# Kernel optimization log

Hardware: AMD Instinct MI355X
Metric: run time of the kernel (lower is better)

Reference implementation:

```python
import jax, jax.numpy as jnp
import numpy as np

NU, NI, E = 100000, 100000, 500000  # users, items, edges per edge type
DIN, DH, DOUT = 128, 256, 128


def setup_inputs() -> dict:
    key = jax.random.key(0)
    ks = jax.random.split(key, 18)
    f = lambda k, s: jax.random.normal(k, s, dtype=jnp.float32) * 0.02
    inp = {
        # node embedding tables (x_dict defaults to embedding weights)
        'emb_user': f(ks[0], (NU, DIN)),
        'emb_item': f(ks[1], (NI, DIN)),
        # conv1 params: relation user->item (dst=item) and item->user (dst=user)
        'W1_self_ui': f(ks[2], (DIN, DH)), 'W1_neigh_ui': f(ks[3], (DIN, DH)), 'b1_ui': jnp.zeros((DH,), jnp.float32),
        'W1_self_iu': f(ks[4], (DIN, DH)), 'W1_neigh_iu': f(ks[5], (DIN, DH)), 'b1_iu': jnp.zeros((DH,), jnp.float32),
        # conv2 params
        'W2_self_ui': f(ks[6], (DH, DOUT)), 'W2_neigh_ui': f(ks[7], (DH, DOUT)), 'b2_ui': jnp.zeros((DOUT,), jnp.float32),
        'W2_self_iu': f(ks[8], (DH, DOUT)), 'W2_neigh_iu': f(ks[9], (DH, DOUT)), 'b2_iu': jnp.zeros((DOUT,), jnp.float32),
        # edge lists: e1 = user->item edges, e2 = item->user edges
        'e1_src': jax.random.randint(ks[10], (E,), 0, NU),
        'e1_dst': jax.random.randint(ks[11], (E,), 0, NI),
        'e2_src': jax.random.randint(ks[12], (E,), 0, NI),
        'e2_dst': jax.random.randint(ks[13], (E,), 0, NU),
    }
    return inp


def _sage(h_src, h_dst, e_src, e_dst, W_self, W_neigh, b, n_dst):
    # DGL SAGEConv('mean'): fc_self(h_dst) + fc_neigh(mean_neighbors(h_src)) + bias
    msg = h_src[e_src]                                   # [E, d] gather
    ssum = jax.ops.segment_sum(msg, e_dst, num_segments=n_dst)          # [n_dst, d]
    deg = jax.ops.segment_sum(jnp.ones((e_src.shape[0], 1), h_src.dtype), e_dst, num_segments=n_dst)
    mean = ssum / jnp.maximum(deg, 1.0)                  # zero in-degree -> 0
    return h_dst @ W_self + mean @ W_neigh + b


def reference(emb_user, emb_item,
              W1_self_ui, W1_neigh_ui, b1_ui, W1_self_iu, W1_neigh_iu, b1_iu,
              W2_self_ui, W2_neigh_ui, b2_ui, W2_self_iu, W2_neigh_iu, b2_iu,
              e1_src, e1_dst, e2_src, e2_dst):
    # layer 1 (HeteroGraphConv: each ntype receives from exactly one relation)
    h1_item = jax.nn.leaky_relu(_sage(emb_user, emb_item, e1_src, e1_dst, W1_self_ui, W1_neigh_ui, b1_ui, NI))
    h1_user = jax.nn.leaky_relu(_sage(emb_item, emb_user, e2_src, e2_dst, W1_self_iu, W1_neigh_iu, b1_iu, NU))
    # layer 2
    h2_item = _sage(h1_user, h1_item, e1_src, e1_dst, W2_self_ui, W2_neigh_ui, b2_ui, NI)
    h2_user = _sage(h1_item, h1_user, e2_src, e2_dst, W2_self_iu, W2_neigh_iu, b2_iu, NU)
    return (h2_user, h2_item)
```

## Files before the change

### kernel.cpp

```cpp
#include <hip/hip_runtime.h>
#include <stdint.h>

typedef unsigned short u16;
typedef unsigned int   u32;
typedef __attribute__((ext_vector_type(8))) short bf16x8;
typedef __attribute__((ext_vector_type(4))) float f32x4;
typedef __attribute__((ext_vector_type(2))) float f32x2;
typedef __attribute__((ext_vector_type(8))) unsigned short u16x8;

constexpr int NUc = 100000;
constexpr int NIc = 100000;
constexpr int Ec  = 500000;
constexpr int Mrows = 100000;
constexpr int NB  = (100000 + 255) / 256;

__device__ __forceinline__ u16 f2bf(float f) {
  u32 u = __float_as_uint(f);
  u += 0x7fffu + ((u >> 16) & 1u);
  return (u16)(u >> 16);
}

__global__ void hist_kernel(const int* __restrict__ e1_dst, const int* __restrict__ e2_dst,
                            int* __restrict__ ideg1, int* __restrict__ ideg2,
                            int* __restrict__ rank1, int* __restrict__ rank2) {
  int i = blockIdx.x * blockDim.x + threadIdx.x;
  const int stride = gridDim.x * blockDim.x;
  for (; i < 2 * Ec; i += stride) {
    if (i < Ec) rank1[i] = atomicAdd(&ideg1[e1_dst[i]], 1);
    else        rank2[i - Ec] = atomicAdd(&ideg2[e2_dst[i - Ec]], 1);
  }
}

constexpr int PREP_B = 4096;
__global__ void prep_cast(const float* __restrict__ eu, const float* __restrict__ ei,
                          const float* __restrict__ W1s_ui, const float* __restrict__ W1n_ui,
                          const float* __restrict__ W1s_iu, const float* __restrict__ W1n_iu,
                          const float* __restrict__ W2s_ui, const float* __restrict__ W2n_ui,
                          const float* __restrict__ W2s_iu, const float* __restrict__ W2n_iu,
                          u16* __restrict__ ue, u16* __restrict__ ie,
                          u16* __restrict__ Wt1_ui, u16* __restrict__ Wt1_iu,
                          u16* __restrict__ Wt2c_u, u16* __restrict__ Wt2c_i) {
  constexpr int N4 = NUc * 128 / 4;
  constexpr int TOT = 2 * N4 + 262144;
  int i = blockIdx.x * blockDim.x + threadIdx.x;
  const int stride = PREP_B * 256;
  for (int t = i; t < TOT; t += stride) {
    if (t < 2 * N4) {
      const float* src = (t < N4) ? eu : ei;
      u16* dst = (t < N4) ? ue : ie;
      int c = (t < N4) ? t : t - N4;
      f32x4 v = __builtin_nontemporal_load(reinterpret_cast<const f32x4*>(src) + c);
      ushort4 o;
      o.x = f2bf(v.x); o.y = f2bf(v.y); o.z = f2bf(v.z); o.w = f2bf(v.w);
      reinterpret_cast<ushort4*>(dst)[c] = o;
    } else {
      int j = t - 2 * N4;
      if (j < 131072) {
        const float* Ws = (j < 65536) ? W1s_ui : W1s_iu;
        const float* Wn = (j < 65536) ? W1n_ui : W1n_iu;
        u16* dst = (j < 65536) ? Wt1_ui : Wt1_iu;
        int q = j & 65535;
        int n = q >> 8, k = q & 255;
        dst[q] = f2bf(k < 128 ? Ws[k * 256 + n] : Wn[(k - 128) * 256 + n]);
      } else {
        int q = j - 131072;
        int which = q >> 16;
        int s = q & 65535;
        int c = s >> 8, k = s & 255;
        float v;
        if (which == 0) v = (c < 128) ? W2n_ui[k * 128 + c] : W2s_iu[k * 128 + (c - 128)];
        else            v = (c < 128) ? W2n_iu[k * 128 + c] : W2s_ui[k * 128 + (c - 128)];
        u16* dst = which ? Wt2c_i : Wt2c_u;
        dst[s] = f2bf(v);
      }
    }
  }
}

__global__ void block_reduce2(const int* __restrict__ ideg1, const int* __restrict__ ideg2,
                              int* __restrict__ bsum1, int* __restrict__ bsum2, int n) {
  const int* deg = blockIdx.y ? ideg2 : ideg1;
  int* bsum = blockIdx.y ? bsum2 : bsum1;
  __shared__ int s[256];
  int t = threadIdx.x, i = blockIdx.x * 256 + t;
  s[t] = (i < n) ? deg[i] : 0;
  __syncthreads();
  for (int st = 128; st > 0; st >>= 1) { if (t < st) s[t] += s[t + st]; __syncthreads(); }
  if (t == 0) bsum[blockIdx.x] = s[0];
}

__global__ void scan_bsums2(const int* __restrict__ bsum1, const int* __restrict__ bsum2,
                            int* __restrict__ bscan1, int* __restrict__ bscan2, int nb) {
  const int* bsum = blockIdx.x ? bsum2 : bsum1;
  int* bscan = blockIdx.x ? bscan2 : bscan1;
  __shared__ int s[512];
  int t = threadIdx.x;
  int v0 = (t < nb) ? bsum[t] : 0;
  s[t] = v0;
  __syncthreads();
  for (int d = 1; d < 512; d <<= 1) {
    int v = (t >= d) ? s[t - d] : 0;
    __syncthreads();
    s[t] += v;
    __syncthreads();
  }
  if (t < nb) bscan[t] = s[t] - v0;
}

__global__ void scan_blocks2(const int* __restrict__ ideg1, const int* __restrict__ ideg2,
                             const int* __restrict__ bscan1, const int* __restrict__ bscan2,
                             int* __restrict__ off1, int* __restrict__ off2, int n) {
  const int* deg = blockIdx.y ? ideg2 : ideg1;
  const int* bscan = blockIdx.y ? bscan2 : bscan1;
  int* off = blockIdx.y ? off2 : off1;
  __shared__ int s[256];
  int t = threadIdx.x, i = blockIdx.x * 256 + t;
  int d = (i < n) ? deg[i] : 0;
  s[t] = d;
  __syncthreads();
  for (int st = 1; st < 256; st <<= 1) {
    int v = (t >= st) ? s[t - st] : 0;
    __syncthreads();
    s[t] += v;
    __syncthreads();
  }
  if (i < n) off[i] = bscan[blockIdx.x] + s[t] - d;
  if (i == 0) off[n] = Ec;
}

__global__ void fill_csr_kernel(const int* __restrict__ e1_src, const int* __restrict__ e1_dst,
                                const int* __restrict__ e2_src, const int* __restrict__ e2_dst,
                                const int* __restrict__ rank1, const int* __restrict__ rank2,
                                const int* __restrict__ off1, const int* __restrict__ off2,
                                int* __restrict__ csr1, int* __restrict__ csr2) {
  int i = blockIdx.x * blockDim.x + threadIdx.x;
  const int stride = gridDim.x * blockDim.x;
  for (; i < 2 * Ec; i += stride) {
    if (i < Ec) {
      int d = __builtin_nontemporal_load(e1_dst + i);
      int r = __builtin_nontemporal_load(rank1 + i);
      csr1[off1[d] + r] = __builtin_nontemporal_load(e1_src + i);
    } else {
      int e = i - Ec;
      int d = __builtin_nontemporal_load(e2_dst + e);
      int r = __builtin_nontemporal_load(rank2 + e);
      csr2[off2[d] + r] = __builtin_nontemporal_load(e2_src + e);
    }
  }
}

template<int FINAL>
__global__ __launch_bounds__(256) void gather_blk(
    const u16* __restrict__ fA, const int* __restrict__ offA, const int* __restrict__ csrA,
    const u16* __restrict__ sA, void* __restrict__ outA,
    const u16* __restrict__ fB, const int* __restrict__ offB, const int* __restrict__ csrB,
    const u16* __restrict__ sB, void* __restrict__ outB)
{
  constexpr int ROWS = 64;
  constexpr int CAP  = 1536;
  constexpr int NBLK = (100000 + ROWS - 1) / ROWS;
  __shared__ int s_off[ROWS + 1];
  __shared__ int s_csr[CAP];

  const int b = blockIdx.x;
  const u16* f; const int* off; const int* csr; const u16* sf; void* out; int r0;
  if (b < NBLK) { f = fA; off = offA; csr = csrA; sf = sA; out = outA; r0 = b * ROWS; }
  else          { f = fB; off = offB; csr = csrB; sf = sB; out = outB; r0 = (b - NBLK) * ROWS; }

  const int tid = threadIdx.x;
  if (tid <= ROWS) s_off[tid] = off[min(r0 + tid, 100000)];
  __syncthreads();
  const int j0 = s_off[0];
  const int nE = s_off[ROWS] - j0;
  const bool inLds = (nE <= CAP);
  if (inLds) {
    for (int j = tid; j < nE; j += 256) s_csr[j] = csr[j0 + j];
  }
  __syncthreads();

  const int w = tid >> 6, lane = tid & 63;
  const int colb = lane << 1;
  for (int rr = w; rr < ROWS; rr += 4) {
    const int r = r0 + rr;
    if (r >= 100000) break;
    const int a0 = s_off[rr], a1 = s_off[rr + 1];
    float ax = 0.f, ay = 0.f;
    if (inLds) {
      int tl = a0 - j0;
      const int el = a1 - j0;
      for (; tl + 4 <= el; tl += 4) {
        int s0 = s_csr[tl], s1 = s_csr[tl + 1], s2 = s_csr[tl + 2], s3 = s_csr[tl + 3];
        u32 v0 = *reinterpret_cast<const u32*>(f + (size_t)s0 * 128 + colb);
        u32 v1 = *reinterpret_cast<const u32*>(f + (size_t)s1 * 128 + colb);
        u32 v2 = *reinterpret_cast<const u32*>(f + (size_t)s2 * 128 + colb);
        u32 v3 = *reinterpret_cast<const u32*>(f + (size_t)s3 * 128 + colb);
        ax += __uint_as_float(v0 << 16) + __uint_as_float(v1 << 16)
            + __uint_as_float(v2 << 16) + __uint_as_float(v3 << 16);
        ay += __uint_as_float(v0 & 0xffff0000u) + __uint_as_float(v1 & 0xffff0000u)
            + __uint_as_float(v2 & 0xffff0000u) + __uint_as_float(v3 & 0xffff0000u);
      }
      for (; tl < el; ++tl) {
        int s0 = s_csr[tl];
        u32 v0 = *reinterpret_cast<const u32*>(f + (size_t)s0 * 128 + colb);
        ax += __uint_as_float(v0 << 16);
        ay += __uint_as_float(v0 & 0xffff0000u);
      }
    } else {
      int t = a0;
      for (; t + 4 <= a1; t += 4) {
        int s0 = csr[t], s1 = csr[t + 1], s2 = csr[t + 2], s3 = csr[t + 3];
        u32 v0 = *reinterpret_cast<const u32*>(f + (size_t)s0 * 128 + colb);
        u32 v1 = *reinterpret_cast<const u32*>(f + (size_t)s1 * 128 + colb);
        u32 v2 = *reinterpret_cast<const u32*>(f + (size_t)s2 * 128 + colb);
        u32 v3 = *reinterpret_cast<const u32*>(f + (size_t)s3 * 128 + colb);
        ax += __uint_as_float(v0 << 16) + __uint_as_float(v1 << 16)
            + __uint_as_float(v2 << 16) + __uint_as_float(v3 << 16);
        ay += __uint_as_float(v0 & 0xffff0000u) + __uint_as_float(v1 & 0xffff0000u)
            + __uint_as_float(v2 & 0xffff0000u) + __uint_as_float(v3 & 0xffff0000u);
      }
      for (; t < a1; ++t) {
        int s0 = csr[t];
        u32 v0 = *reinterpret_cast<const u32*>(f + (size_t)s0 * 128 + colb);
        ax += __uint_as_float(v0 << 16);
        ay += __uint_as_float(v0 & 0xffff0000u);
      }
    }
    float rs = 1.0f / fmaxf((float)(a1 - a0), 1.0f);
    if (FINAL) {
      u32 sv = __builtin_nontemporal_load(
          reinterpret_cast<const u32*>(sf + (size_t)r * 128 + colb));
      f32x2 o;
      o.x = ax * rs + __uint_as_float(sv << 16);
      o.y = ay * rs + __uint_as_float(sv & 0xffff0000u);
      __builtin_nontemporal_store(o, reinterpret_cast<f32x2*>((float*)out + (size_t)r * 128 + colb));
    } else {
      u32 o = (u32)f2bf(ax * rs) | ((u32)f2bf(ay * rs) << 16);
      *reinterpret_cast<u32*>((u16*)out + (size_t)r * 128 + colb) = o;
    }
  }
}

__device__ __forceinline__ void glds16(const void* g, void* l) {
  __builtin_amdgcn_global_load_lds((const __attribute__((address_space(1))) void*)g,
                                   (__attribute__((address_space(3))) void*)l, 16, 0, 0);
}

__global__ __launch_bounds__(256) void fused_gemm(
    const u16* __restrict__ Xa, const u16* __restrict__ Sa,
    const u16* __restrict__ W1a, const float* __restrict__ b1a,
    const u16* __restrict__ W2a, const float* __restrict__ b2a,
    u16* __restrict__ proja, u16* __restrict__ selfa,
    const u16* __restrict__ Xb, const u16* __restrict__ Sb,
    const u16* __restrict__ W1b, const float* __restrict__ b1b,
    const u16* __restrict__ W2b, const float* __restrict__ b2b,
    u16* __restrict__ projb, u16* __restrict__ selfb,
    int M)
{
  constexpr int K = 256, BK = 32, BM = 64;
  __shared__ __align__(16) u16 As[BM * BK];
  __shared__ __align__(16) u16 Bs[256 * BK];
  __shared__ __align__(16) u16 slab[BM * 256];

  const bool zb = (blockIdx.z != 0);
  const u16* X   = zb ? Xb : Xa;
  const u16* S   = zb ? Sb : Sa;
  const u16* W1  = zb ? W1b : W1a;
  const float* b1 = zb ? b1b : b1a;
  const u16* W2  = zb ? W2b : W2a;
  const float* b2 = zb ? b2b : b2a;
  u16* proj  = zb ? projb : proja;
  u16* selfp = zb ? selfb : selfa;

  const int tid  = threadIdx.x;
  const int lane = tid & 63;
  const int w    = tid >> 6;
  const int gr0  = blockIdx.x * BM;
  const int rl   = tid >> 2;
  const int sslot = tid & 3;

  f32x4 acc[4][4];
  #pragma unroll
  for (int m = 0; m < 4; ++m)
    #pragma unroll
    for (int n = 0; n < 4; ++n) acc[m][n] = (f32x4){0.f, 0.f, 0.f, 0.f};

  for (int kt = 0; kt < K; kt += BK) {
    const u16* At = (kt >= 128) ? S : X;
    const int kbase = kt & 127;
    {
      int swz = (sslot ^ ((rl >> 1) & 3)) << 3;
      int grow = gr0 + rl; grow = grow < M ? grow : M - 1;
      glds16(At + (size_t)grow * 128 + kbase + swz, As + (size_t)(w * 16) * BK);
    }
    #pragma unroll
    for (int h = 0; h < 4; ++h) {
      int rb = h * 64 + rl;
      int swz = (sslot ^ ((rb >> 1) & 3)) << 3;
      glds16(W1 + (size_t)rb * K + kt + swz, Bs + (size_t)(h * 64 + w * 16) * BK);
    }
    __syncthreads();

    bf16x8 af[4], bfr[4];
    #pragma unroll
    for (int m = 0; m < 4; ++m) {
      int row = m * 16 + (lane & 15);
      int idx = (row << 5) + ((((lane >> 4) ^ ((row >> 1) & 3))) << 3);
      af[m] = *reinterpret_cast<const bf16x8*>(As + idx);
    }
    #pragma unroll
    for (int n = 0; n < 4; ++n) {
      int row = w * 64 + n * 16 + (lane & 15);
      int idx = (row << 5) + ((((lane >> 4) ^ ((row >> 1) & 3))) << 3);
      bfr[n] = *reinterpret_cast<const bf16x8*>(Bs + idx);
    }
    #pragma unroll
    for (int m = 0; m < 4; ++m)
      #pragma unroll
      for (int n = 0; n < 4; ++n)
        acc[m][n] = __builtin_amdgcn_mfma_f32_16x16x32_bf16(af[m], bfr[n], acc[m][n], 0, 0, 0);
    __syncthreads();
  }

  #pragma unroll
  for (int n = 0; n < 4; ++n) {
    int c = w * 64 + n * 16 + (lane & 15);
    float b = b1[c];
    #pragma unroll
    for (int m = 0; m < 4; ++m) {
      #pragma unroll
      for (int r = 0; r < 4; ++r) {
        int row = m * 16 + ((lane >> 4) << 2) + r;
        float v = acc[m][n][r] + b;
        v = (v >= 0.f) ? v : 0.01f * v;
        int g = (c >> 3) ^ (row & 7);
        slab[row * 256 + g * 8 + (c & 7)] = f2bf(v);
        acc[m][n][r] = 0.f;
      }
    }
  }
  __syncthreads();

  for (int kt = 0; kt < K; kt += BK) {
    #pragma unroll
    for (int h = 0; h < 4; ++h) {
      int rb = h * 64 + rl;
      int swz = (sslot ^ ((rb >> 1) & 3)) << 3;
      glds16(W2 + (size_t)rb * K + kt + swz, Bs + (size_t)(h * 64 + w * 16) * BK);
    }
    __syncthreads();

    bf16x8 af[4], bfr[4];
    #pragma unroll
    for (int m = 0; m < 4; ++m) {
      int row = m * 16 + (lane & 15);
      int g = ((kt >> 3) + (lane >> 4)) ^ (row & 7);
      af[m] = *reinterpret_cast<const bf16x8*>(slab + row * 256 + g * 8);
    }
    #pragma unroll
    for (int n = 0; n < 4; ++n) {
      int row = w * 64 + n * 16 + (lane & 15);
      int idx = (row << 5) + ((((lane >> 4) ^ ((row >> 1) & 3))) << 3);
      bfr[n] = *reinterpret_cast<const bf16x8*>(Bs + idx);
    }
    #pragma unroll
    for (int m = 0; m < 4; ++m)
      #pragma unroll
      for (int n = 0; n < 4; ++n)
        acc[m][n] = __builtin_amdgcn_mfma_f32_16x16x32_bf16(af[m], bfr[n], acc[m][n], 0, 0, 0);
    __syncthreads();
  }

  #pragma unroll
  for (int n = 0; n < 4; ++n) {
    int c = w * 64 + n * 16 + (lane & 15);
    float b = (c >= 128) ? b2[c - 128] : 0.f;
    #pragma unroll
    for (int m = 0; m < 4; ++m) {
      #pragma unroll
      for (int r = 0; r < 4; ++r) {
        int row = m * 16 + ((lane >> 4) << 2) + r;
        int g = (c >> 3) ^ (row & 7);
        slab[row * 256 + g * 8 + (c & 7)] = f2bf(acc[m][n][r] + b);
      }
    }
  }
  __syncthreads();
  #pragma unroll
  for (int p = 0; p < 8; ++p) {
    int chunk = p * 256 + tid;
    int row = chunk >> 5;
    int gg  = chunk & 31;
    int G = gr0 + row;
    if (G < M) {
      int gsw = gg ^ (row & 7);
      u16x8 v = *reinterpret_cast<const u16x8*>(slab + row * 256 + gsw * 8);
      int col = gg * 8;
      if (col < 128)
        *reinterpret_cast<u16x8*>(proj + (size_t)G * 128 + col) = v;
      else
        __builtin_nontemporal_store(v,
            reinterpret_cast<u16x8*>(selfp + (size_t)G * 128 + (col - 128)));
    }
  }
}

extern "C" void kernel_launch(void* const* d_in, const int* in_sizes, int n_in,
                              void* d_out, int out_size, void* d_ws, size_t ws_size,
                              hipStream_t stream) {
  const float* emb_user    = (const float*)d_in[0];
  const float* emb_item    = (const float*)d_in[1];
  const float* W1_self_ui  = (const float*)d_in[2];
  const float* W1_neigh_ui = (const float*)d_in[3];
  const float* b1_ui       = (const float*)d_in[4];
  const float* W1_self_iu  = (const float*)d_in[5];
  const float* W1_neigh_iu = (const float*)d_in[6];
  const float* b1_iu       = (const float*)d_in[7];
  const float* W2_self_ui  = (const float*)d_in[8];
  const float* W2_neigh_ui = (const float*)d_in[9];
  const float* b2_ui       = (const float*)d_in[10];
  const float* W2_self_iu  = (const float*)d_in[11];
  const float* W2_neigh_iu = (const float*)d_in[12];
  const float* b2_iu       = (const float*)d_in[13];
  const int* e1_src = (const int*)d_in[14];
  const int* e1_dst = (const int*)d_in[15];
  const int* e2_src = (const int*)d_in[16];
  const int* e2_dst = (const int*)d_in[17];

  u16* p16 = (u16*)d_ws;
  u16* ue       = p16; p16 += (size_t)NUc * 128;
  u16* ie       = p16; p16 += (size_t)NIc * 128;
  u16* aggb_i   = p16; p16 += (size_t)NIc * 128;
  u16* aggb_u   = p16; p16 += (size_t)NUc * 128;
  u16* proj_u2i = p16; p16 += (size_t)NUc * 128;
  u16* self_u   = p16; p16 += (size_t)NUc * 128;
  u16* proj_i2u = p16; p16 += (size_t)NIc * 128;
  u16* self_i   = p16; p16 += (size_t)NIc * 128;
  u16* Wt1_ui   = p16; p16 += 256 * 256;
  u16* Wt1_iu   = p16; p16 += 256 * 256;
  u16* Wt2c_u   = p16; p16 += 256 * 256;
  u16* Wt2c_i   = p16; p16 += 256 * 256;
  int* ip    = (int*)p16;
  int* ideg1 = ip;  ip += NIc;
  int* ideg2 = ip;  ip += NUc;
  int* off1  = ip;  ip += NIc + 1;
  int* off2  = ip;  ip += NUc + 1;
  int* rank1 = ip;  ip += Ec;
  int* rank2 = ip;  ip += Ec;
  int* csr1  = ip;  ip += Ec;
  int* csr2  = ip;  ip += Ec;
  int* bsum1 = ip;  ip += 512;
  int* bscan1= ip;  ip += 512;
  int* bsum2 = ip;  ip += 512;
  int* bscan2= ip;  ip += 512;

  float* h2_user = (float*)d_out;
  float* h2_item = h2_user + (size_t)NUc * 128;

  dim3 blk(256);
  const int gatherBlocks = 2 * ((100000 + 63) / 64);
  dim3 fusedGrid((100000 + 63) / 64, 1, 2);

  hipMemsetAsync(ideg1, 0, sizeof(int) * (size_t)(NIc + NUc), stream);
  hist_kernel<<<1024, blk, 0, stream>>>(e1_dst, e2_dst, ideg1, ideg2, rank1, rank2);
  prep_cast<<<PREP_B, blk, 0, stream>>>(
      emb_user, emb_item,
      W1_self_ui, W1_neigh_ui, W1_self_iu, W1_neigh_iu,
      W2_self_ui, W2_neigh_ui, W2_self_iu, W2_neigh_iu,
      ue, ie, Wt1_ui, Wt1_iu, Wt2c_u, Wt2c_i);
  block_reduce2<<<dim3(NB, 2), blk, 0, stream>>>(ideg1, ideg2, bsum1, bsum2, NIc);
  scan_bsums2<<<2, 512, 0, stream>>>(bsum1, bsum2, bscan1, bscan2, NB);
  scan_blocks2<<<dim3(NB, 2), blk, 0, stream>>>(ideg1, ideg2, bscan1, bscan2, off1, off2, NIc);
  fill_csr_kernel<<<1024, blk, 0, stream>>>(e1_src, e1_dst, e2_src, e2_dst,
                                            rank1, rank2, off1, off2, csr1, csr2);

  gather_blk<0><<<gatherBlocks, blk, 0, stream>>>(
      ue, off1, csr1, nullptr, aggb_i,
      ie, off2, csr2, nullptr, aggb_u);

  fused_gemm<<<fusedGrid, blk, 0, stream>>>(
      ie, aggb_i, Wt1_ui, b1_ui, Wt2c_i, b2_ui, proj_i2u, self_i,
      ue, aggb_u, Wt1_iu, b1_iu, Wt2c_u, b2_iu, proj_u2i, self_u, Mrows);

  gather_blk<1><<<gatherBlocks, blk, 0, stream>>>(
      proj_u2i, off1, csr1, self_i, h2_item,
      proj_i2u, off2, csr2, self_u, h2_user);
}
```

Before: 342.1 us.

## Double-buffer LDS tiles in fused GEMM to overlap loads with MFMA

```diff
diff --git a/kernel.cpp b/kernel.cpp
--- a/kernel.cpp
+++ b/kernel.cpp
@@ -257,8 +257,10 @@
     int M)
 {
   constexpr int K = 256, BK = 32, BM = 64;
-  __shared__ __align__(16) u16 As[BM * BK];
-  __shared__ __align__(16) u16 Bs[256 * BK];
+  __shared__ __align__(16) u16 As0[BM * BK];
+  __shared__ __align__(16) u16 Bs0[256 * BK];
+  __shared__ __align__(16) u16 As1[BM * BK];
+  __shared__ __align__(16) u16 Bs1[256 * BK];
   __shared__ __align__(16) u16 slab[BM * 256];
 
   const bool zb = (blockIdx.z != 0);
@@ -278,40 +280,58 @@
   const int rl   = tid >> 2;
   const int sslot = tid & 3;
 
+  const int aswz = (sslot ^ ((rl >> 1) & 3)) << 3;
+  int grow = gr0 + rl; grow = grow < M ? grow : M - 1;
+  const size_t arow = (size_t)grow * 128 + aswz;
+
+  auto stageA1 = [&](int kt, u16* Asb) {
+    const u16* At = (kt >= 128) ? S : X;
+    glds16(At + arow + (kt & 127), Asb + (size_t)(w * 16) * BK);
+  };
+  auto stageB = [&](const u16* W, int kt, u16* Bsb) {
+    #pragma unroll
+    for (int h = 0; h < 4; ++h) {
+      int rb = h * 64 + rl;
+      int swz = (sslot ^ ((rb >> 1) & 3)) << 3;
+      glds16(W + (size_t)rb * K + kt + swz, Bsb + (size_t)(h * 64 + w * 16) * BK);
+    }
+  };
+
   f32x4 acc[4][4];
   #pragma unroll
   for (int m = 0; m < 4; ++m)
     #pragma unroll
     for (int n = 0; n < 4; ++n) acc[m][n] = (f32x4){0.f, 0.f, 0.f, 0.f};
 
+  stageA1(0, As0);
+  stageB(W1, 0, Bs0);
+  __syncthreads();
+
+  int db = 0;
   for (int kt = 0; kt < K; kt += BK) {
-    const u16* At = (kt >= 128) ? S : X;
-    const int kbase = kt & 127;
-    {
-      int swz = (sslot ^ ((rl >> 1) & 3)) << 3;
-      int grow = gr0 + rl; grow = grow < M ? grow : M - 1;
-      glds16(At + (size_t)grow * 128 + kbase + swz, As + (size_t)(w * 16) * BK);
-    }
-    #pragma unroll
-    for (int h = 0; h < 4; ++h) {
-      int rb = h * 64 + rl;
-      int swz = (sslot ^ ((rb >> 1) & 3)) << 3;
-      glds16(W1 + (size_t)rb * K + kt + swz, Bs + (size_t)(h * 64 + w * 16) * BK);
-    }
-    __syncthreads();
+    u16* AsN = db ? As0 : As1;
+    u16* BsN = db ? Bs0 : Bs1;
+    if (kt + BK < K) {
+      stageA1(kt + BK, AsN);
+      stageB(W1, kt + BK, BsN);
+    } else {
+      stageB(W2, 0, BsN);
+    }
+    const u16* Asb = db ? As1 : As0;
+    const u16* Bsb = db ? Bs1 : Bs0;
 
     bf16x8 af[4], bfr[4];
     #pragma unroll
     for (int m = 0; m < 4; ++m) {
       int row = m * 16 + (lane & 15);
       int idx = (row << 5) + ((((lane >> 4) ^ ((row >> 1) & 3))) << 3);
-      af[m] = *reinterpret_cast<const bf16x8*>(As + idx);
+      af[m] = *reinterpret_cast<const bf16x8*>(Asb + idx);
     }
     #pragma unroll
     for (int n = 0; n < 4; ++n) {
       int row = w * 64 + n * 16 + (lane & 15);
       int idx = (row << 5) + ((((lane >> 4) ^ ((row >> 1) & 3))) << 3);
-      bfr[n] = *reinterpret_cast<const bf16x8*>(Bs + idx);
+      bfr[n] = *reinterpret_cast<const bf16x8*>(Bsb + idx);
     }
     #pragma unroll
     for (int m = 0; m < 4; ++m)
@@ -319,6 +339,7 @@
       for (int n = 0; n < 4; ++n)
         acc[m][n] = __builtin_amdgcn_mfma_f32_16x16x32_bf16(af[m], bfr[n], acc[m][n], 0, 0, 0);
     __syncthreads();
+    db ^= 1;
   }
 
   #pragma unroll
@@ -341,13 +362,9 @@
   __syncthreads();
 
   for (int kt = 0; kt < K; kt += BK) {
-    #pragma unroll
-    for (int h = 0; h < 4; ++h) {
-      int rb = h * 64 + rl;
-      int swz = (sslot ^ ((rb >> 1) & 3)) << 3;
-      glds16(W2 + (size_t)rb * K + kt + swz, Bs + (size_t)(h * 64 + w * 16) * BK);
-    }
-    __syncthreads();
+    u16* BsN = db ? Bs0 : Bs1;
+    if (kt + BK < K) stageB(W2, kt + BK, BsN);
+    const u16* Bsb = db ? Bs1 : Bs0;
 
     bf16x8 af[4], bfr[4];
     #pragma unroll
@@ -360,7 +377,7 @@
     for (int n = 0; n < 4; ++n) {
       int row = w * 64 + n * 16 + (lane & 15);
       int idx = (row << 5) + ((((lane >> 4) ^ ((row >> 1) & 3))) << 3);
-      bfr[n] = *reinterpret_cast<const bf16x8*>(Bs + idx);
+      bfr[n] = *reinterpret_cast<const bf16x8*>(Bsb + idx);
     }
     #pragma unroll
     for (int m = 0; m < 4; ++m)
@@ -368,6 +385,7 @@
       for (int n = 0; n < 4; ++n)
         acc[m][n] = __builtin_amdgcn_mfma_f32_16x16x32_bf16(af[m], bfr[n], acc[m][n], 0, 0, 0);
     __syncthreads();
+    db ^= 1;
   }
 
   #pragma unroll
```

After: 338.6 us (median of 2 runs). About the same (-1.0%).
